# Performance work log

Hardware: AMD Instinct MI355X
Metric: run time of the kernel (lower is better)

The kernel has to match this reference:

```python
import jax, jax.numpy as jnp
import numpy as np

B, C, N = 8, 20, 2000
IOU_THR = 0.5      # module default iou=0.5 when iou_threshold is None
SCORE_THR = 0.1    # score threshold (module default 0.0; see notes)


def setup_inputs() -> dict:
    key = jax.random.key(0)
    k1, k2 = jax.random.split(key)
    # two random corner points per box -> valid boxes in [y1,x1,y2,x2] (ONNX default layout)
    pts = jax.random.uniform(k1, (B, N, 2, 2), dtype=jnp.float32)
    lo = jnp.min(pts, axis=2)
    hi = jnp.max(pts, axis=2)
    boxes = jnp.stack([lo[..., 0], lo[..., 1], hi[..., 0], hi[..., 1]], axis=-1)  # [B,N,4]
    scores = jax.random.uniform(k2, (B, C, N), dtype=jnp.float32)
    return {"boxes": boxes, "scores": scores}


def _pairwise_iou(b):
    # b: [B, N, 4] in x1,y1,x2,y2
    x1, y1, x2, y2 = b[..., 0], b[..., 1], b[..., 2], b[..., 3]
    area = (x2 - x1) * (y2 - y1)                                  # [B,N]
    ix1 = jnp.maximum(x1[:, :, None], x1[:, None, :])
    iy1 = jnp.maximum(y1[:, :, None], y1[:, None, :])
    ix2 = jnp.minimum(x2[:, :, None], x2[:, None, :])
    iy2 = jnp.minimum(y2[:, :, None], y2[:, None, :])
    inter = jnp.clip(ix2 - ix1, 0.0) * jnp.clip(iy2 - iy1, 0.0)   # [B,N,N]
    union = area[:, :, None] + area[:, None, :] - inter
    return inter / jnp.maximum(union, 1e-9)


def _nms_one(iou_b, scores_bc):
    # iou_b: [N,N] shared per image; scores_bc: [N] one class
    n = scores_bc.shape[0]
    valid = scores_bc > SCORE_THR
    # sort descending by score; invalid boxes pushed to the end
    order = jnp.argsort(jnp.where(valid, -scores_bc, jnp.inf))    # [N]
    keep0 = valid[order]
    idx = jnp.arange(n)

    def body(i, keep):
        row = iou_b[order[i]][order]                               # IoU of i-th sorted box vs all (sorted)
        sup = (row > IOU_THR) & (idx > i) & keep[i]
        return keep & ~sup

    keep = jax.lax.fori_loop(0, n, body, keep0)
    return order, keep


def reference(boxes, scores):
    b, c, n = scores.shape
    # center_point_box == 0: [y1,x1,y2,x2] -> [x1,y1,x2,y2]
    conv = boxes[..., jnp.array([1, 0, 3, 2])]
    iou = _pairwise_iou(conv)                                      # [B,N,N]
    nms_classes = jax.vmap(_nms_one, in_axes=(None, 0))            # over classes
    order, keep = jax.vmap(nms_classes, in_axes=(0, 0))(iou, scores)  # [B,C,N] each
    bidx = jnp.broadcast_to(jnp.arange(b)[:, None, None], (b, c, n))
    cidx = jnp.broadcast_to(jnp.arange(c)[None, :, None], (b, c, n))
    triples = jnp.stack([bidx, cidx, order], axis=-1).astype(jnp.int32)  # [B,C,N,3]
    # fixed-shape padded output: rows not kept are marked -1 (jit-compatible variant of (num_selected,3))
    return jnp.where(keep[..., None], triples, jnp.int32(-1))
```

## Files before the change

kernel.cpp:

```cpp
#include <hip/hip_runtime.h>
#include <stdint.h>

#define NB 8
#define NC 20
#define NN 2000
#define NP 2048
#define NBLK 32
#define RG 125
#define IOU_THR 0.5f
#define SCORE_THR 0.1f

__global__ __launch_bounds__(256) void k_iou_bits(const float* __restrict__ boxes,
                                                  uint32_t* __restrict__ rowbits) {
#pragma clang fp contract(off)
    int b = blockIdx.x / RG;
    int g = blockIdx.x % RG;
    __shared__ float4 bx[NP];
    __shared__ float ars[NP];
    for (int j = threadIdx.x; j < NP; j += 256) {
        float4 v = make_float4(0.f, 0.f, 0.f, 0.f);
        if (j < NN) {
            const float4 p = *reinterpret_cast<const float4*>(boxes + ((size_t)b * NN + j) * 4);
            v = make_float4(p.y, p.x, p.w, p.z);
        }
        bx[j] = v;
        ars[j] = (v.z - v.x) * (v.w - v.y);
    }
    __syncthreads();
    int wave = threadIdx.x >> 6;
    int lane = threadIdx.x & 63;
    for (int rr = 0; rr < 4; ++rr) {
        int i = g * 16 + wave * 4 + rr;
        float4 bi = bx[i];
        float ai = ars[i];
        uint32_t myword = 0;
        for (int jj = 0; jj < 32; ++jj) {
            int j = jj * 64 + lane;
            float4 bj = bx[j];
            float aj = ars[j];
            float ix1 = fmaxf(bi.x, bj.x);
            float iy1 = fmaxf(bi.y, bj.y);
            float ix2 = fminf(bi.z, bj.z);
            float iy2 = fminf(bi.w, bj.w);
            float iw = fmaxf(ix2 - ix1, 0.0f);
            float ih = fmaxf(iy2 - iy1, 0.0f);
            float inter = iw * ih;
            float uni = (ai + aj) - inter;
            float iou = inter / fmaxf(uni, 1e-9f);
            bool sup = iou > IOU_THR;
            unsigned long long m = __ballot(sup);
            if ((lane >> 1) == jj)
                myword = (lane & 1) ? (uint32_t)(m >> 32) : (uint32_t)m;
        }
        rowbits[((size_t)b * NN + i) * 64 + lane] = myword;
    }
}

__global__ __launch_bounds__(1024) void k_sort(const float* __restrict__ scores,
                                               uint64_t* __restrict__ skeys) {
    int bc = blockIdx.x;
    __shared__ uint64_t keys[NP];
    const float* sc = scores + (size_t)bc * NN;
    for (int i = threadIdx.x; i < NP; i += 1024) {
        uint64_t k;
        if (i < NN) {
            float s = sc[i];
            uint32_t hi = (s > SCORE_THR) ? (0xFFFFFFFFu - __float_as_uint(s))
                                          : 0xFFFFFFFFu;
            k = ((uint64_t)hi << 32) | (uint32_t)i;
        } else {
            k = ~0ull;
        }
        keys[i] = k;
    }
    __syncthreads();
    for (int k = 2; k <= NP; k <<= 1) {
        for (int j = k >> 1; j > 0; j >>= 1) {
            for (int idx = threadIdx.x; idx < NP; idx += 1024) {
                int l = idx ^ j;
                if (l > idx) {
                    uint64_t a = keys[idx], bb = keys[l];
                    bool up = ((idx & k) == 0);
                    if ((a > bb) == up) { keys[idx] = bb; keys[l] = a; }
                }
            }
            __syncthreads();
        }
    }
    for (int i = threadIdx.x; i < NN; i += 1024)
        skeys[(size_t)bc * NN + i] = keys[i];
}

__global__ __launch_bounds__(64) void k_nms(const uint64_t* __restrict__ skeys,
                                            const uint32_t* __restrict__ rowbits,
                                            int* __restrict__ out) {
    __shared__ uint32_t rows[2][64 * 64];
    int bid = blockIdx.x;
    int b = bid & 7;
    int c = bid >> 3;
    int bc = b * NC + c;
    int lane = threadIdx.x;
    const uint32_t* rb = rowbits + (size_t)b * NN * 64;
    const uint64_t* sk = skeys + (size_t)bc * NN;
    int* o = out + (size_t)bc * NN * 3;
    uint32_t removed = 0;
    uint32_t keptacc = 0;

    uint64_t kcur = sk[lane];
    {
        uint32_t ordp = (uint32_t)kcur;
#pragma unroll
        for (int q = 0; q < 16; ++q) {
            uint32_t oo = (uint32_t)__shfl((int)ordp, q * 4 + (lane >> 4));
            const uint32_t* g = rb + (size_t)oo * 64 + (size_t)((lane & 15) * 4);
            __builtin_amdgcn_global_load_lds(
                (const __attribute__((address_space(1))) void*)g,
                (__attribute__((address_space(3))) void*)(&rows[0][0] + q * 256),
                16, 0, 0);
        }
    }
    uint64_t knext = ~0ull;
    { int i1 = 64 + lane; if (i1 < NN) knext = sk[i1]; }

    for (int bk = 0; bk < NBLK; ++bk) {
        asm volatile("s_waitcnt vmcnt(0)" ::: "memory");

        if (bk + 1 < NBLK) {
            int inx = (bk + 1) * 64 + lane;
            uint32_t ordp = (inx < NN) ? (uint32_t)knext : 0u;
            uint32_t* lb = &rows[(bk + 1) & 1][0];
#pragma unroll
            for (int q = 0; q < 16; ++q) {
                uint32_t oo = (uint32_t)__shfl((int)ordp, q * 4 + (lane >> 4));
                const uint32_t* g = rb + (size_t)oo * 64 + (size_t)((lane & 15) * 4);
                __builtin_amdgcn_global_load_lds(
                    (const __attribute__((address_space(1))) void*)g,
                    (__attribute__((address_space(3))) void*)(lb + q * 256),
                    16, 0, 0);
            }
        }
        uint64_t kfut = ~0ull;
        if (bk + 2 < NBLK) {
            int i2 = (bk + 2) * 64 + lane;
            if (i2 < NN) kfut = sk[i2];
        }

        const uint32_t* lrow = &rows[bk & 1][0];
        int i = bk * 64 + lane;
        bool inb = i < NN;
        uint32_t ord = (uint32_t)kcur;
        bool valid = inb && ((uint32_t)(kcur >> 32) != 0xFFFFFFFFu);
        uint32_t osafe = valid ? ord : 0u;
        uint32_t ws = osafe >> 5, bs = osafe & 31;
        uint32_t w = (uint32_t)__shfl((int)removed, (int)ws);
        bool alive0 = valid && !((w >> bs) & 1u);

        const uint32_t* myw = lrow + ws;
        uint32_t lo = 0, hi = 0;
#pragma unroll
        for (int u = 0; u < 32; ++u) {
            uint32_t wrd = myw[u * 64];
            lo |= ((wrd >> bs) & 1u) << u;
        }
#pragma unroll
        for (int u = 0; u < 32; ++u) {
            uint32_t wrd = myw[(u + 32) * 64];
            hi |= ((wrd >> bs) & 1u) << u;
        }
        uint64_t sup = ((uint64_t)hi << 32) | lo;
        sup &= (1ull << lane) - 1ull;

        unsigned long long undec = __ballot(alive0);
        uint64_t kept64 = 0ull;
        while (undec) {
            bool mine  = (undec >> lane) & 1ull;
            bool ready = mine && ((sup & undec) == 0ull);
            bool kp    = ready && ((sup & kept64) == 0ull);
            unsigned long long readym = __ballot(ready);
            unsigned long long kpm    = __ballot(kp);
            kept64 |= kpm;
            undec &= ~readym;
        }

        uint64_t km = kept64;
        while (km) {
            int u = __builtin_ctzll(km);
            km &= km - 1;
            removed |= lrow[(unsigned)u * 64 + lane];
        }
        if ((kept64 >> lane) & 1ull) keptacc |= 1u << bk;
        kcur = knext;
        knext = kfut;
    }

    for (int bk = 0; bk < NBLK; ++bk) {
        int i = bk * 64 + lane;
        if (i < NN) {
            uint32_t ord = (uint32_t)sk[i];
            bool kept = (keptacc >> bk) & 1u;
            int base = i * 3;
            o[base + 0] = kept ? b : -1;
            o[base + 1] = kept ? c : -1;
            o[base + 2] = kept ? (int)ord : -1;
        }
    }
}

extern "C" void kernel_launch(void* const* d_in, const int* in_sizes, int n_in,
                              void* d_out, int out_size, void* d_ws, size_t ws_size,
                              hipStream_t stream) {
    (void)in_sizes; (void)n_in; (void)out_size; (void)ws_size;
    const float* boxes  = (const float*)d_in[0];
    const float* scores = (const float*)d_in[1];
    int* out = (int*)d_out;

    uint32_t* rowbits = (uint32_t*)d_ws;
    uint64_t* skeys   = (uint64_t*)((char*)d_ws +
                                    (size_t)NB * NN * 64 * sizeof(uint32_t));

    k_iou_bits<<<dim3(NB * RG), dim3(256), 0, stream>>>(boxes, rowbits);
    k_sort   <<<dim3(NB * NC), dim3(1024), 0, stream>>>(scores, skeys);
    k_nms    <<<dim3(NB * NC), dim3(64),  0, stream>>>(skeys, rowbits, out);
}
```

Before: 194.7 us.

## Register-resident bitonic sort with wavefront shuffles; batch LDS row loads in NMS

Rewrites the per-class bitonic sort so each thread keeps two keys in registers. Only stages with stride of 128 or more go through shared memory with barriers; smaller strides use wavefront xor-shuffles and stride 1 is an in-register compare-swap. This removes most __syncthreads and LDS traffic from the sort. Separately, the NMS kernel loads all 64 row words into a register array before extracting bits, and sets launch bounds to one block per CU so the higher register use is allowed.

```diff
diff --git a/kernel.cpp b/kernel.cpp
--- a/kernel.cpp
+++ b/kernel.cpp
@@ -56,44 +56,58 @@
     }
 }
 
+__device__ __forceinline__ uint64_t sort_key(const float* sc, int i) {
+    if (i < NN) {
+        float s = sc[i];
+        uint32_t hi = (s > SCORE_THR) ? (0xFFFFFFFFu - __float_as_uint(s))
+                                      : 0xFFFFFFFFu;
+        return ((uint64_t)hi << 32) | (uint32_t)i;
+    }
+    return ~0ull;
+}
+
 __global__ __launch_bounds__(1024) void k_sort(const float* __restrict__ scores,
                                                uint64_t* __restrict__ skeys) {
     int bc = blockIdx.x;
+    int t = threadIdx.x;
     __shared__ uint64_t keys[NP];
     const float* sc = scores + (size_t)bc * NN;
-    for (int i = threadIdx.x; i < NP; i += 1024) {
-        uint64_t k;
-        if (i < NN) {
-            float s = sc[i];
-            uint32_t hi = (s > SCORE_THR) ? (0xFFFFFFFFu - __float_as_uint(s))
-                                          : 0xFFFFFFFFu;
-            k = ((uint64_t)hi << 32) | (uint32_t)i;
-        } else {
-            k = ~0ull;
-        }
-        keys[i] = k;
-    }
-    __syncthreads();
+    uint64_t e0 = sort_key(sc, 2 * t);
+    uint64_t e1 = sort_key(sc, 2 * t + 1);
+
     for (int k = 2; k <= NP; k <<= 1) {
         for (int j = k >> 1; j > 0; j >>= 1) {
-            for (int idx = threadIdx.x; idx < NP; idx += 1024) {
-                int l = idx ^ j;
-                if (l > idx) {
-                    uint64_t a = keys[idx], bb = keys[l];
-                    bool up = ((idx & k) == 0);
-                    if ((a > bb) == up) { keys[idx] = bb; keys[l] = a; }
-                }
+            bool up = (((2 * t) & k) == 0);
+            if (j >= 128) {
+                keys[2 * t] = e0;
+                keys[2 * t + 1] = e1;
+                __syncthreads();
+                uint64_t p0 = keys[(2 * t) ^ j];
+                uint64_t p1 = keys[(2 * t + 1) ^ j];
+                bool lower = (((2 * t) & j) == 0);
+                e0 = (lower == up) ? (e0 < p0 ? e0 : p0) : (e0 > p0 ? e0 : p0);
+                e1 = (lower == up) ? (e1 < p1 ? e1 : p1) : (e1 > p1 ? e1 : p1);
+                __syncthreads();
+            } else if (j >= 2) {
+                int m = j >> 1;
+                uint64_t p0 = __shfl_xor((unsigned long long)e0, m, 64);
+                uint64_t p1 = __shfl_xor((unsigned long long)e1, m, 64);
+                bool lower = ((t & m) == 0);
+                e0 = (lower == up) ? (e0 < p0 ? e0 : p0) : (e0 > p0 ? e0 : p0);
+                e1 = (lower == up) ? (e1 < p1 ? e1 : p1) : (e1 > p1 ? e1 : p1);
+            } else {
+                if (up ? (e0 > e1) : (e0 < e1)) { uint64_t tmp = e0; e0 = e1; e1 = tmp; }
             }
-            __syncthreads();
-        }
-    }
-    for (int i = threadIdx.x; i < NN; i += 1024)
-        skeys[(size_t)bc * NN + i] = keys[i];
-}
-
-__global__ __launch_bounds__(64) void k_nms(const uint64_t* __restrict__ skeys,
-                                            const uint32_t* __restrict__ rowbits,
-                                            int* __restrict__ out) {
+        }
+    }
+    int i0 = 2 * t;
+    if (i0 < NN)     skeys[(size_t)bc * NN + i0] = e0;
+    if (i0 + 1 < NN) skeys[(size_t)bc * NN + i0 + 1] = e1;
+}
+
+__global__ __launch_bounds__(64, 1) void k_nms(const uint64_t* __restrict__ skeys,
+                                               const uint32_t* __restrict__ rowbits,
+                                               int* __restrict__ out) {
     __shared__ uint32_t rows[2][64 * 64];
     int bid = blockIdx.x;
     int b = bid & 7;
@@ -156,17 +170,14 @@
         bool alive0 = valid && !((w >> bs) & 1u);
 
         const uint32_t* myw = lrow + ws;
+        uint32_t wv[64];
+#pragma unroll
+        for (int u = 0; u < 64; ++u) wv[u] = myw[u * 64];
         uint32_t lo = 0, hi = 0;
 #pragma unroll
-        for (int u = 0; u < 32; ++u) {
-            uint32_t wrd = myw[u * 64];
-            lo |= ((wrd >> bs) & 1u) << u;
-        }
-#pragma unroll
-        for (int u = 0; u < 32; ++u) {
-            uint32_t wrd = myw[(u + 32) * 64];
-            hi |= ((wrd >> bs) & 1u) << u;
-        }
+        for (int u = 0; u < 32; ++u) lo |= ((wv[u] >> bs) & 1u) << u;
+#pragma unroll
+        for (int u = 0; u < 32; ++u) hi |= ((wv[u + 32] >> bs) & 1u) << u;
         uint64_t sup = ((uint64_t)hi << 32) | lo;
         sup &= (1ull << lane) - 1ull;
 
```

Result: faster. 180.4 us (-7.3%).
